# Kernel optimization log

Hardware: AMD Instinct MI355X
Metric: run time of the kernel (lower is better)

Reference implementation:

```python
import jax, jax.numpy as jnp
import numpy as np

D_MODEL = 1024
N_HEADS = 16
HEAD_DIM = D_MODEL // N_HEADS


def setup_inputs() -> dict:
    key = jax.random.key(0)
    k_x, k_wqkv, k_bqkv, k_wo, k_bo = jax.random.split(key, 5)
    lim_qkv = 1.0 / np.sqrt(D_MODEL)
    return {
        "x": jax.random.normal(k_x, (2, 4096, D_MODEL), dtype=jnp.float32),
        "w_qkv": jax.random.uniform(k_wqkv, (D_MODEL, 3 * D_MODEL), minval=-lim_qkv, maxval=lim_qkv, dtype=jnp.float32),
        "b_qkv": jax.random.uniform(k_bqkv, (3 * D_MODEL,), minval=-lim_qkv, maxval=lim_qkv, dtype=jnp.float32),
        "w_out": jax.random.uniform(k_wo, (D_MODEL, D_MODEL), minval=-lim_qkv, maxval=lim_qkv, dtype=jnp.float32),
        "b_out": jax.random.uniform(k_bo, (D_MODEL,), minval=-lim_qkv, maxval=lim_qkv, dtype=jnp.float32),
    }


def reference(x, w_qkv, b_qkv, w_out, b_out):
    b, s, _ = x.shape
    scale = HEAD_DIM ** -0.5
    qkv = x @ w_qkv + b_qkv                              # [b, s, 3*d]
    qkv = qkv.reshape(b, s, 3, N_HEADS, HEAD_DIM)
    qkv = jnp.transpose(qkv, (2, 0, 3, 1, 4))            # [3, b, h, s, hd]
    q, k, v = qkv[0], qkv[1], qkv[2]
    scores = jnp.einsum("bhqd,bhkd->bhqk", q, k) * scale  # [b, h, s, s]
    causal = jnp.triu(jnp.ones((s, s), dtype=bool), k=1)
    scores = jnp.where(causal, -jnp.inf, scores)
    probs = jax.nn.softmax(scores, axis=-1)
    out = jnp.einsum("bhqk,bhkd->bhqd", probs, v)         # [b, h, s, hd]
    out = jnp.transpose(out, (0, 2, 1, 3)).reshape(b, s, D_MODEL)
    return out @ w_out + b_out
```

## Files before the change

### kernel.cpp

```cpp
#include <hip/hip_runtime.h>
#include <math.h>

#define S_LEN 4096
#define DM    1024
#define NHEAD 16
#define HDIM  64
#define C3    3072

typedef __attribute__((ext_vector_type(8))) short bf8_t;
typedef __attribute__((ext_vector_type(4))) float f32x4;
typedef __attribute__((ext_vector_type(16))) float f32x16;

__device__ __forceinline__ short f2bf(float f) {
    union { float f; unsigned u; } v; v.f = f;
    unsigned r = v.u + 0x7FFF + ((v.u >> 16) & 1);
    return (short)(r >> 16);
}
__device__ __forceinline__ float fexp2(float x) { return __builtin_amdgcn_exp2f(x); }

__device__ __forceinline__ unsigned cvtpk(float a, float b) {
    unsigned r;
    asm("v_cvt_pk_bf16_f32 %0, %1, %2" : "=v"(r) : "v"(a), "v"(b));
    return r;
}

__device__ __forceinline__ void gload_lds16(const void* g, void* l) {
    __builtin_amdgcn_global_load_lds(
        (const __attribute__((address_space(1))) unsigned int*)g,
        (__attribute__((address_space(3))) unsigned int*)l, 16, 0, 0);
}

__device__ __forceinline__ float vmax16(f32x16 s) {
    float a = fmaxf(fmaxf(s[0], s[1]), s[2]);
    float b = fmaxf(fmaxf(s[3], s[4]), s[5]);
    float c = fmaxf(fmaxf(s[6], s[7]), s[8]);
    float d = fmaxf(fmaxf(s[9], s[10]), s[11]);
    float e = fmaxf(fmaxf(s[12], s[13]), s[14]);
    float f = fmaxf(fmaxf(a, b), s[15]);
    float g = fmaxf(fmaxf(c, d), e);
    return fmaxf(f, g);
}
__device__ __forceinline__ float vsum16(f32x16 s) {
    float a = (s[0] + s[1]) + (s[2] + s[3]);
    float b = (s[4] + s[5]) + (s[6] + s[7]);
    float c = (s[8] + s[9]) + (s[10] + s[11]);
    float d = (s[12] + s[13]) + (s[14] + s[15]);
    return (a + b) + (c + d);
}

__global__ void cast_f32_bf16(const float* __restrict__ in, short* __restrict__ out, int n8)
{
    int i = blockIdx.x * blockDim.x + threadIdx.x;
    if (i < n8) {
        float4 a = ((const float4*)in)[i * 2];
        float4 b = ((const float4*)in)[i * 2 + 1];
        bf8_t v = {f2bf(a.x), f2bf(a.y), f2bf(a.z), f2bf(a.w),
                   f2bf(b.x), f2bf(b.y), f2bf(b.z), f2bf(b.w)};
        ((bf8_t*)out)[i] = v;
    }
}

__global__ __launch_bounds__(256)
void transpose_cast(const float* __restrict__ in, short* __restrict__ out, int R, int C)
{
    __shared__ float t[32][33];
    const int tx = threadIdx.x & 31;
    const int ty = threadIdx.x >> 5;
    const int r0 = blockIdx.y * 32;
    const int c0 = blockIdx.x * 32;
    #pragma unroll
    for (int i = 0; i < 32; i += 8)
        t[ty + i][tx] = in[(size_t)(r0 + ty + i) * C + c0 + tx];
    __syncthreads();
    #pragma unroll
    for (int i = 0; i < 32; i += 8)
        out[(size_t)(c0 + ty + i) * R + r0 + tx] = f2bf(t[tx][ty + i]);
}

__global__ __launch_bounds__(256)
void transpose_v(const short* __restrict__ qkv, short* __restrict__ vt)
{
    __shared__ short t[64][72];
    const int st = blockIdx.x, bh = blockIdx.y;
    const int b = bh >> 4, h = bh & 15;
    const int tid = threadIdx.x;
    const int r   = tid >> 2;
    const int c16 = (tid & 3) * 16;
    const short* src = qkv + (size_t)b * S_LEN * C3 + 2 * DM + h * HDIM;
    const short* sp  = src + (size_t)(st * 64 + r) * C3 + c16;
    *(bf8_t*)&t[r][c16]     = *(const bf8_t*)sp;
    *(bf8_t*)&t[r][c16 + 8] = *(const bf8_t*)(sp + 8);
    __syncthreads();
    short tmp[16];
    #pragma unroll
    for (int i = 0; i < 16; ++i) tmp[i] = t[c16 + i][r];
    short* dp = vt + (size_t)bh * HDIM * S_LEN + (size_t)r * S_LEN + st * 64 + c16;
    *(bf8_t*)dp       = *(bf8_t*)&tmp[0];
    *(bf8_t*)(dp + 8) = *(bf8_t*)&tmp[8];
}

template<bool BF16OUT>
__global__ __launch_bounds__(256)
void gemm_mfma(const short* __restrict__ A, const short* __restrict__ Bt,
               const float* __restrict__ bias, void* __restrict__ Cout,
               int M, int N)
{
    constexpr int K = 1024;
    __shared__ __align__(16) short As[128 * 64];
    __shared__ __align__(16) short Bs[128 * 64];

    const int nbx = N / 128;
    const int nwg = (M / 128) * nbx;
    int bid = blockIdx.x;
    bid = (bid & 7) * (nwg >> 3) + (bid >> 3);
    const int by = bid / nbx, bx = bid % nbx;
    const int row0 = by * 128, col0 = bx * 128;

    const int tid  = threadIdx.x;
    const int lane = tid & 63;
    const int w    = tid >> 6;
    const int l15  = lane & 15;
    const int l4   = lane >> 4;
    const int wr   = w >> 1, wc = w & 1;

    f32x4 acc[4][4];
    #pragma unroll
    for (int i = 0; i < 4; ++i)
        #pragma unroll
        for (int j = 0; j < 4; ++j) acc[i][j] = (f32x4){0.f, 0.f, 0.f, 0.f};

    size_t goff[4];
    int    loff[4];
    #pragma unroll
    for (int i = 0; i < 4; ++i) {
        const int o   = (w * 4 + i) * 1024 + lane * 16;
        const int row = o >> 7;
        const int col = (o & 127) ^ ((row & 7) << 4);
        goff[i] = (size_t)row * (K * 2) + col;
        loff[i] = o;
    }
    const char* Ab = (const char*)A  + (size_t)row0 * (K * 2);
    const char* Bb = (const char*)Bt + (size_t)col0 * (K * 2);

    for (int k0 = 0; k0 < K; k0 += 64) {
        __syncthreads();
        #pragma unroll
        for (int i = 0; i < 4; ++i) {
            gload_lds16(Ab + goff[i] + k0 * 2, (char*)As + loff[i]);
            gload_lds16(Bb + goff[i] + k0 * 2, (char*)Bs + loff[i]);
        }
        __syncthreads();

        #pragma unroll
        for (int ks = 0; ks < 2; ++ks) {
            bf8_t af[4], bfr[4];
            #pragma unroll
            for (int mi = 0; mi < 4; ++mi) {
                const int row = wr * 64 + mi * 16 + l15;
                const int off = (row * 128 + ks * 64 + l4 * 16) ^ ((row & 7) << 4);
                af[mi] = *(bf8_t*)((char*)As + off);
            }
            #pragma unroll
            for (int ni = 0; ni < 4; ++ni) {
                const int row = wc * 64 + ni * 16 + l15;
                const int off = (row * 128 + ks * 64 + l4 * 16) ^ ((row & 7) << 4);
                bfr[ni] = *(bf8_t*)((char*)Bs + off);
            }
            #pragma unroll
            for (int mi = 0; mi < 4; ++mi)
                #pragma unroll
                for (int ni = 0; ni < 4; ++ni)
                    acc[mi][ni] = __builtin_amdgcn_mfma_f32_16x16x32_bf16(
                        af[mi], bfr[ni], acc[mi][ni], 0, 0, 0);
        }
    }

    float bv[4];
    #pragma unroll
    for (int ni = 0; ni < 4; ++ni)
        bv[ni] = bias[col0 + wc * 64 + ni * 16 + l15];

    #pragma unroll
    for (int mi = 0; mi < 4; ++mi)
        #pragma unroll
        for (int r = 0; r < 4; ++r) {
            const int row = row0 + wr * 64 + mi * 16 + l4 * 4 + r;
            #pragma unroll
            for (int ni = 0; ni < 4; ++ni) {
                const int col = col0 + wc * 64 + ni * 16 + l15;
                const float val = acc[mi][ni][r] + bv[ni];
                if constexpr (BF16OUT)
                    ((short*)Cout)[(size_t)row * N + col] = f2bf(val);
                else
                    ((float*)Cout)[(size_t)row * N + col] = val;
            }
        }
}

__global__ __launch_bounds__(256)
void attn_mfma32(const short* __restrict__ qkv, const short* __restrict__ vt,
                 short* __restrict__ out)
{
    const int g   = blockIdx.x;
    const int bh  = blockIdx.y;
    const int b   = bh >> 4, h = bh & 15;
    const int tid = threadIdx.x;
    const int lane = tid & 63;
    const int w    = tid >> 6;
    const int l31  = lane & 31;
    const int hi   = lane >> 5;

    __shared__ __align__(16) short lds[2][2][64 * 64];

    const float C   = 0.125f * 1.44269504f;
    const float NEG = -1e30f;
    const float THR = 40.0f;

    const short* qkb = qkv + (size_t)b * S_LEN * C3 + h * HDIM;

    const int sr = tid >> 3;
    const int sc = ((tid & 7) * 16) ^ ((sr & 7) << 4);
    const char* srcK = (const char*)(qkb + DM) + (size_t)sr * (C3 * 2) + sc;
    const char* srcV = (const char*)(vt + (size_t)bh * HDIM * S_LEN)
                       + (size_t)sr * (S_LEN * 2) + sc;
    const int ldst = tid * 16;

    #pragma unroll 1
    for (int half = 0; half < 2; ++half) {
        const int qb     = half ? g : (31 - g);
        const int Q0     = qb * 128;
        const int nkt    = qb * 2 + 2;
        const int qmin_w = Q0 + w * 32;
        const int qmax_w = qmin_w + 31;
        const int q_g    = qmin_w + l31;
        const int nkt_w  = (qmax_w >> 6) + 1;

        bf8_t qf[4];
        {
            const short* qp = qkb + (size_t)q_g * C3 + hi * 8;
            qf[0] = *(const bf8_t*)(qp);
            qf[1] = *(const bf8_t*)(qp + 16);
            qf[2] = *(const bf8_t*)(qp + 32);
            qf[3] = *(const bf8_t*)(qp + 48);
        }

        f32x16 o0, o1;
        #pragma unroll
        for (int r = 0; r < 16; ++r) { o0[r] = 0.f; o1[r] = 0.f; }
        float m = NEG, l = 0.f;

        gload_lds16(srcK,                     (char*)lds + ldst);
        gload_lds16(srcK + 32 * (C3 * 2),     (char*)lds + 4096 + ldst);
        gload_lds16(srcV,                     (char*)lds + 8192 + ldst);
        gload_lds16(srcV + 32 * (S_LEN * 2),  (char*)lds + 12288 + ldst);
        __syncthreads();

        for (int kt = 0; kt < nkt; ++kt) {
            const int cur = kt & 1;
            if (kt + 1 < nkt) {
                const char* sK = srcK + (size_t)(kt + 1) * 64 * (C3 * 2);
                const char* sV = srcV + (size_t)(kt + 1) * 64 * 2;
                char* dstb = (char*)lds + (cur ^ 1) * 16384;
                gload_lds16(sK,                    dstb + ldst);
                gload_lds16(sK + 32 * (C3 * 2),    dstb + 4096 + ldst);
                gload_lds16(sV,                    dstb + 8192 + ldst);
                gload_lds16(sV + 32 * (S_LEN * 2), dstb + 12288 + ldst);
            }

            if (kt < nkt_w) {
                const char* Kb = (char*)lds + cur * 16384;
                const char* Vb = Kb + 8192;
                const int kb0 = kt * 64;
                const bool act1 = (kb0 + 32) <= qmax_w;

                f32x16 s0, s1;
                #pragma unroll
                for (int r = 0; r < 16; ++r) { s0[r] = 0.f; s1[r] = NEG; }
                __builtin_amdgcn_s_setprio(1);
                #pragma unroll
                for (int ds = 0; ds < 4; ++ds) {
                    const int R0 = l31;
                    const int off0 = (R0 * 128 + ds * 32 + hi * 16) ^ ((R0 & 7) << 4);
                    bf8_t kf = *(const bf8_t*)(Kb + off0);
                    s0 = __builtin_amdgcn_mfma_f32_32x32x16_bf16(kf, qf[ds], s0, 0, 0, 0);
                }
                if (act1) {
                    #pragma unroll
                    for (int r = 0; r < 16; ++r) s1[r] = 0.f;
                    #pragma unroll
                    for (int ds = 0; ds < 4; ++ds) {
                        const int R1 = 32 + l31;
                        const int off1 = (R1 * 128 + ds * 32 + hi * 16) ^ ((R1 & 7) << 4);
                        bf8_t kf = *(const bf8_t*)(Kb + off1);
                        s1 = __builtin_amdgcn_mfma_f32_32x32x16_bf16(kf, qf[ds], s1, 0, 0, 0);
                    }
                }
                __builtin_amdgcn_s_setprio(0);

                if (kb0 + 31 > qmin_w) {
                    #pragma unroll
                    for (int r = 0; r < 16; ++r) {
                        const int k = kb0 + 4 * hi + ((r & 3) + 8 * (r >> 2));
                        if (k > q_g) s0[r] = NEG;
                    }
                }
                if (act1 && (kb0 + 63 > qmin_w)) {
                    #pragma unroll
                    for (int r = 0; r < 16; ++r) {
                        const int k = kb0 + 32 + 4 * hi + ((r & 3) + 8 * (r >> 2));
                        if (k > q_g) s1[r] = NEG;
                    }
                }

                float tm = fmaxf(vmax16(s0), vmax16(s1));
                tm = fmaxf(tm, __shfl_xor(tm, 32));

                if (!__all(tm <= m + THR)) {
                    const float mn = fmaxf(m, tm);
                    const float al = fexp2(fmaf(m, C, -mn * C));
                    l *= al;
                    m = mn;
                    #pragma unroll
                    for (int r = 0; r < 16; ++r) {
                        const int cr = 4 * hi + ((r & 3) + 8 * (r >> 2));
                        const float aR = __shfl(al, cr);
                        o0[r] *= aR;
                        o1[r] *= aR;
                    }
                }

                const float cm = m * C;
                #pragma unroll
                for (int r = 0; r < 16; ++r) s0[r] = fexp2(fmaf(s0[r], C, -cm));
                #pragma unroll
                for (int r = 0; r < 16; ++r) s1[r] = fexp2(fmaf(s1[r], C, -cm));

                float rs = vsum16(s0) + vsum16(s1);
                rs += __shfl_xor(rs, 32);
                l += rs;

                unsigned W0[2][4], W1[2][4];
                #pragma unroll
                for (int gg = 0; gg < 4; ++gg) {
                    W0[0][gg] = cvtpk(s0[4 * gg], s0[4 * gg + 1]);
                    W1[0][gg] = cvtpk(s0[4 * gg + 2], s0[4 * gg + 3]);
                    W0[1][gg] = cvtpk(s1[4 * gg], s1[4 * gg + 1]);
                    W1[1][gg] = cvtpk(s1[4 * gg + 2], s1[4 * gg + 3]);
                }

                #pragma unroll
                for (int c = 0; c < 4; ++c) {
                    const int t  = c >> 1;
                    const int gA = 2 * (c & 1);
                    const int gB = gA + 1;
                    const unsigned rx0 = __shfl_xor(hi ? W0[t][gA] : W0[t][gB], 32);
                    const unsigned rx1 = __shfl_xor(hi ? W1[t][gA] : W1[t][gB], 32);
                    union { unsigned u[4]; bf8_t v; } pf;
                    pf.u[0] = hi ? rx0 : W0[t][gA];
                    pf.u[1] = hi ? rx1 : W1[t][gA];
                    pf.u[2] = hi ? W0[t][gB] : rx0;
                    pf.u[3] = hi ? W1[t][gB] : rx1;

                    __builtin_amdgcn_s_setprio(1);
                    {
                        const int R = l31;
                        const int off = (R * 128 + c * 32 + hi * 16) ^ ((R & 7) << 4);
                        bf8_t vf = *(const bf8_t*)(Vb + off);
                        o0 = __builtin_amdgcn_mfma_f32_32x32x16_bf16(pf.v, vf, o0, 0, 0, 0);
                    }
                    {
                        const int R = 32 + l31;
                        const int off = (R * 128 + c * 32 + hi * 16) ^ ((R & 7) << 4);
                        bf8_t vf = *(const bf8_t*)(Vb + off);
                        o1 = __builtin_amdgcn_mfma_f32_32x32x16_bf16(pf.v, vf, o1, 0, 0, 0);
                    }
                    __builtin_amdgcn_s_setprio(0);
                }
            }
            __syncthreads();
        }

        const float inv = 1.f / l;
        #pragma unroll
        for (int r = 0; r < 16; ++r) {
            const int cr = 4 * hi + ((r & 3) + 8 * (r >> 2));
            const float iv = __shfl(inv, cr);
            const int row = Q0 + w * 32 + cr;
            short* op = out + (size_t)(b * S_LEN + row) * DM + h * HDIM + l31;
            op[0]  = f2bf(o0[r] * iv);
            op[32] = f2bf(o1[r] * iv);
        }
    }
}

extern "C" void kernel_launch(void* const* d_in, const int* in_sizes, int n_in,
                              void* d_out, int out_size, void* d_ws, size_t ws_size,
                              hipStream_t stream)
{
    const float* x     = (const float*)d_in[0];
    const float* w_qkv = (const float*)d_in[1];
    const float* b_qkv = (const float*)d_in[2];
    const float* w_out = (const float*)d_in[3];
    const float* b_out = (const float*)d_in[4];
    float* out = (float*)d_out;

    const int M = 2 * S_LEN;

    char* ws = (char*)d_ws;
    short* qkvb  = (short*)(ws);
    short* attnb = (short*)(ws + 50331648);
    short* xb    = (short*)(ws + 67108864);
    short* wqkvT = (short*)(ws + 83886080);
    short* woutT = (short*)(ws + 90177536);
    short* vtb   = (short*)(ws + 92274688);

    cast_f32_bf16<<<dim3((M * DM / 8 + 255) / 256), 256, 0, stream>>>(x, xb, M * DM / 8);
    transpose_cast<<<dim3(C3 / 32, DM / 32), 256, 0, stream>>>(w_qkv, wqkvT, DM, C3);
    transpose_cast<<<dim3(DM / 32, DM / 32), 256, 0, stream>>>(w_out, woutT, DM, DM);

    gemm_mfma<true><<<dim3((M / 128) * (C3 / 128)), 256, 0, stream>>>(
        xb, wqkvT, b_qkv, qkvb, M, C3);

    transpose_v<<<dim3(S_LEN / 64, 2 * NHEAD), 256, 0, stream>>>(qkvb, vtb);

    attn_mfma32<<<dim3(16, 2 * NHEAD), 256, 0, stream>>>(qkvb, vtb, attnb);

    gemm_mfma<false><<<dim3((M / 128) * (DM / 128)), 256, 0, stream>>>(
        attnb, woutT, b_out, out, M, DM);
}
```

Measured before the change: 249.5 us.

## Split attention key tiles across two wave groups with LDS merge of softmax states

The attention block grows from 256 to 512 threads. Each group of four waves handles one 32-key half of every 64-key tile for the same query rows, so each wave runs half the MFMA work per tile and keeps its own running max and sum. At the end, the second group writes its max, sum and partial output to shared memory, and the first group rescales and combines them before writing. This doubles the waves available to hide latency with the same grid, at the cost of extra barriers, an LDS merge step, and possibly fewer resident blocks per CU.

```diff
diff --git a/kernel.cpp b/kernel.cpp
--- a/kernel.cpp
+++ b/kernel.cpp
@@ -197,7 +197,7 @@
         }
 }
 
-__global__ __launch_bounds__(256)
+__global__ __launch_bounds__(512)
 void attn_mfma32(const short* __restrict__ qkv, const short* __restrict__ vt,
                  short* __restrict__ out)
 {
@@ -206,15 +206,18 @@
     const int b   = bh >> 4, h = bh & 15;
     const int tid = threadIdx.x;
     const int lane = tid & 63;
-    const int w    = tid >> 6;
+    const int wv   = tid >> 6;
+    const int w2   = wv & 3;
+    const int s    = wv >> 2;
     const int l31  = lane & 31;
     const int hi   = lane >> 5;
 
     __shared__ __align__(16) short lds[2][2][64 * 64];
 
-    const float C   = 0.125f * 1.44269504f;
-    const float NEG = -1e30f;
-    const float THR = 40.0f;
+    const float C    = 0.125f * 1.44269504f;
+    const float NEGM = -1e30f;
+    const float NEGS = -2e30f;
+    const float THR  = 40.0f;
 
     const short* qkb = qkv + (size_t)b * S_LEN * C3 + h * HDIM;
 
@@ -225,15 +228,18 @@
                        + (size_t)sr * (S_LEN * 2) + sc;
     const int ldst = tid * 16;
 
+    float* mlds = (float*)lds;
+    float* oshr = (float*)lds + 512;
+
     #pragma unroll 1
     for (int half = 0; half < 2; ++half) {
         const int qb     = half ? g : (31 - g);
         const int Q0     = qb * 128;
         const int nkt    = qb * 2 + 2;
-        const int qmin_w = Q0 + w * 32;
+        const int qmin_w = Q0 + w2 * 32;
         const int qmax_w = qmin_w + 31;
         const int q_g    = qmin_w + l31;
-        const int nkt_w  = (qmax_w >> 6) + 1;
+        const int nkt_ws = (qmax_w >= 32 * s) ? (((qmax_w - 32 * s) >> 6) + 1) : 0;
 
         bf8_t qf[4];
         {
@@ -247,12 +253,10 @@
         f32x16 o0, o1;
         #pragma unroll
         for (int r = 0; r < 16; ++r) { o0[r] = 0.f; o1[r] = 0.f; }
-        float m = NEG, l = 0.f;
-
-        gload_lds16(srcK,                     (char*)lds + ldst);
-        gload_lds16(srcK + 32 * (C3 * 2),     (char*)lds + 4096 + ldst);
-        gload_lds16(srcV,                     (char*)lds + 8192 + ldst);
-        gload_lds16(srcV + 32 * (S_LEN * 2),  (char*)lds + 12288 + ldst);
+        float m = NEGM, l = 0.f;
+
+        gload_lds16(srcK, (char*)lds + ldst);
+        gload_lds16(srcV, (char*)lds + 8192 + ldst);
         __syncthreads();
 
         for (int kt = 0; kt < nkt; ++kt) {
@@ -261,39 +265,25 @@
                 const char* sK = srcK + (size_t)(kt + 1) * 64 * (C3 * 2);
                 const char* sV = srcV + (size_t)(kt + 1) * 64 * 2;
                 char* dstb = (char*)lds + (cur ^ 1) * 16384;
-                gload_lds16(sK,                    dstb + ldst);
-                gload_lds16(sK + 32 * (C3 * 2),    dstb + 4096 + ldst);
-                gload_lds16(sV,                    dstb + 8192 + ldst);
-                gload_lds16(sV + 32 * (S_LEN * 2), dstb + 12288 + ldst);
-            }
-
-            if (kt < nkt_w) {
+                gload_lds16(sK, dstb + ldst);
+                gload_lds16(sV, dstb + 8192 + ldst);
+            }
+
+            if (kt < nkt_ws) {
                 const char* Kb = (char*)lds + cur * 16384;
                 const char* Vb = Kb + 8192;
-                const int kb0 = kt * 64;
-                const bool act1 = (kb0 + 32) <= qmax_w;
-
-                f32x16 s0, s1;
-                #pragma unroll
-                for (int r = 0; r < 16; ++r) { s0[r] = 0.f; s1[r] = NEG; }
+                const int kb0 = kt * 64 + 32 * s;
+
+                f32x16 sc_;
+                #pragma unroll
+                for (int r = 0; r < 16; ++r) sc_[r] = 0.f;
                 __builtin_amdgcn_s_setprio(1);
                 #pragma unroll
                 for (int ds = 0; ds < 4; ++ds) {
-                    const int R0 = l31;
-                    const int off0 = (R0 * 128 + ds * 32 + hi * 16) ^ ((R0 & 7) << 4);
+                    const int R0 = 32 * s + l31;
+                    const int off0 = (R0 * 128 + ds * 32 + hi * 16) ^ ((l31 & 7) << 4);
                     bf8_t kf = *(const bf8_t*)(Kb + off0);
-                    s0 = __builtin_amdgcn_mfma_f32_32x32x16_bf16(kf, qf[ds], s0, 0, 0, 0);
-                }
-                if (act1) {
-                    #pragma unroll
-                    for (int r = 0; r < 16; ++r) s1[r] = 0.f;
-                    #pragma unroll
-                    for (int ds = 0; ds < 4; ++ds) {
-                        const int R1 = 32 + l31;
-                        const int off1 = (R1 * 128 + ds * 32 + hi * 16) ^ ((R1 & 7) << 4);
-                        bf8_t kf = *(const bf8_t*)(Kb + off1);
-                        s1 = __builtin_amdgcn_mfma_f32_32x32x16_bf16(kf, qf[ds], s1, 0, 0, 0);
-                    }
+                    sc_ = __builtin_amdgcn_mfma_f32_32x32x16_bf16(kf, qf[ds], sc_, 0, 0, 0);
                 }
                 __builtin_amdgcn_s_setprio(0);
 
@@ -301,18 +291,11 @@
                     #pragma unroll
                     for (int r = 0; r < 16; ++r) {
                         const int k = kb0 + 4 * hi + ((r & 3) + 8 * (r >> 2));
-                        if (k > q_g) s0[r] = NEG;
+                        if (k > q_g) sc_[r] = NEGS;
                     }
                 }
-                if (act1 && (kb0 + 63 > qmin_w)) {
-                    #pragma unroll
-                    for (int r = 0; r < 16; ++r) {
-                        const int k = kb0 + 32 + 4 * hi + ((r & 3) + 8 * (r >> 2));
-                        if (k > q_g) s1[r] = NEG;
-                    }
-                }
-
-                float tm = fmaxf(vmax16(s0), vmax16(s1));
+
+                float tm = vmax16(sc_);
                 tm = fmaxf(tm, __shfl_xor(tm, 32));
 
                 if (!__all(tm <= m + THR)) {
@@ -331,35 +314,31 @@
 
                 const float cm = m * C;
                 #pragma unroll
-                for (int r = 0; r < 16; ++r) s0[r] = fexp2(fmaf(s0[r], C, -cm));
-                #pragma unroll
-                for (int r = 0; r < 16; ++r) s1[r] = fexp2(fmaf(s1[r], C, -cm));
-
-                float rs = vsum16(s0) + vsum16(s1);
+                for (int r = 0; r < 16; ++r) sc_[r] = fexp2(fmaf(sc_[r], C, -cm));
+
+                float rs = vsum16(sc_);
                 rs += __shfl_xor(rs, 32);
                 l += rs;
 
-                unsigned W0[2][4], W1[2][4];
+                unsigned W0[4], W1[4];
                 #pragma unroll
                 for (int gg = 0; gg < 4; ++gg) {
-                    W0[0][gg] = cvtpk(s0[4 * gg], s0[4 * gg + 1]);
-                    W1[0][gg] = cvtpk(s0[4 * gg + 2], s0[4 * gg + 3]);
-                    W0[1][gg] = cvtpk(s1[4 * gg], s1[4 * gg + 1]);
-                    W1[1][gg] = cvtpk(s1[4 * gg + 2], s1[4 * gg + 3]);
+                    W0[gg] = cvtpk(sc_[4 * gg], sc_[4 * gg + 1]);
+                    W1[gg] = cvtpk(sc_[4 * gg + 2], sc_[4 * gg + 3]);
                 }
 
                 #pragma unroll
-                for (int c = 0; c < 4; ++c) {
-                    const int t  = c >> 1;
-                    const int gA = 2 * (c & 1);
+                for (int cl = 0; cl < 2; ++cl) {
+                    const int c  = 2 * s + cl;
+                    const int gA = 2 * cl;
                     const int gB = gA + 1;
-                    const unsigned rx0 = __shfl_xor(hi ? W0[t][gA] : W0[t][gB], 32);
-                    const unsigned rx1 = __shfl_xor(hi ? W1[t][gA] : W1[t][gB], 32);
+                    const unsigned rx0 = __shfl_xor(hi ? W0[gA] : W0[gB], 32);
+                    const unsigned rx1 = __shfl_xor(hi ? W1[gA] : W1[gB], 32);
                     union { unsigned u[4]; bf8_t v; } pf;
-                    pf.u[0] = hi ? rx0 : W0[t][gA];
-                    pf.u[1] = hi ? rx1 : W1[t][gA];
-                    pf.u[2] = hi ? W0[t][gB] : rx0;
-                    pf.u[3] = hi ? W1[t][gB] : rx1;
+                    pf.u[0] = hi ? rx0 : W0[gA];
+                    pf.u[1] = hi ? rx1 : W1[gA];
+                    pf.u[2] = hi ? W0[gB] : rx0;
+                    pf.u[3] = hi ? W1[gB] : rx1;
 
                     __builtin_amdgcn_s_setprio(1);
                     {
@@ -380,16 +359,52 @@
             __syncthreads();
         }
 
-        const float inv = 1.f / l;
-        #pragma unroll
-        for (int r = 0; r < 16; ++r) {
-            const int cr = 4 * hi + ((r & 3) + 8 * (r >> 2));
-            const float iv = __shfl(inv, cr);
-            const int row = Q0 + w * 32 + cr;
-            short* op = out + (size_t)(b * S_LEN + row) * DM + h * HDIM + l31;
-            op[0]  = f2bf(o0[r] * iv);
-            op[32] = f2bf(o1[r] * iv);
-        }
+        float inv = 0.f, a0q = 0.f, a1q = 0.f;
+        if (s) {
+            mlds[(w2 * 2 + 0) * 64 + lane] = m;
+            mlds[(w2 * 2 + 1) * 64 + lane] = l;
+            #pragma unroll
+            for (int r = 0; r < 16; ++r)
+                oshr[(w2 * 16 + r) * 64 + lane] = o0[r];
+        }
+        __syncthreads();
+        if (!s) {
+            const float m1 = mlds[(w2 * 2 + 0) * 64 + lane];
+            const float l1 = mlds[(w2 * 2 + 1) * 64 + lane];
+            const float ms = fmaxf(m, m1);
+            a0q = fexp2(fmaf(m,  C, -ms * C));
+            a1q = fexp2(fmaf(m1, C, -ms * C));
+            inv = 1.f / (a0q * l + a1q * l1);
+            #pragma unroll
+            for (int r = 0; r < 16; ++r) {
+                const int cr = 4 * hi + ((r & 3) + 8 * (r >> 2));
+                const float a0r = __shfl(a0q, cr);
+                const float a1r = __shfl(a1q, cr);
+                o0[r] = a0r * o0[r] + a1r * oshr[(w2 * 16 + r) * 64 + lane];
+            }
+        }
+        __syncthreads();
+        if (s) {
+            #pragma unroll
+            for (int r = 0; r < 16; ++r)
+                oshr[(w2 * 16 + r) * 64 + lane] = o1[r];
+        }
+        __syncthreads();
+        if (!s) {
+            #pragma unroll
+            for (int r = 0; r < 16; ++r) {
+                const int cr = 4 * hi + ((r & 3) + 8 * (r >> 2));
+                const float a0r = __shfl(a0q, cr);
+                const float a1r = __shfl(a1q, cr);
+                const float iv  = __shfl(inv, cr);
+                const float v1  = a0r * o1[r] + a1r * oshr[(w2 * 16 + r) * 64 + lane];
+                const int row = Q0 + w2 * 32 + cr;
+                short* op = out + (size_t)(b * S_LEN + row) * DM + h * HDIM + l31;
+                op[0]  = f2bf(o0[r] * iv);
+                op[32] = f2bf(v1 * iv);
+            }
+        }
+        __syncthreads();
     }
 }
 
@@ -423,7 +438,7 @@
 
     transpose_v<<<dim3(S_LEN / 64, 2 * NHEAD), 256, 0, stream>>>(qkvb, vtb);
 
-    attn_mfma32<<<dim3(16, 2 * NHEAD), 256, 0, stream>>>(qkvb, vtb, attnb);
+    attn_mfma32<<<dim3(16, 2 * NHEAD), 512, 0, stream>>>(qkvb, vtb, attnb);
 
     gemm_mfma<false><<<dim3((M / 128) * (DM / 128)), 256, 0, stream>>>(
         attnb, woutT, b_out, out, M, DM);
```

New measurement: 270.1 us. 8.3% more time.
